# Optimization experiments

Hardware: AMD Instinct MI355X
Metric: run time of the kernel (lower is better)

Reference implementation:

```python
import jax, jax.numpy as jnp
import numpy as np

N_NODES = 50000
N_EDGES = 800000
IN_FEAT = 256
OUT_FEAT = 256
NUM_RELS = 8
ALPHA = 0.5


def setup_inputs() -> dict:
    key = jax.random.key(0)
    k1, k2, k3, k4, k5, k6 = jax.random.split(key, 6)
    x = jax.random.normal(k1, (N_NODES, IN_FEAT), dtype=jnp.float32)
    edge_index = jax.random.randint(k2, (2, N_EDGES), 0, N_NODES, dtype=jnp.int64)
    edge_type = jax.random.randint(k3, (N_EDGES,), 0, NUM_RELS, dtype=jnp.int64)
    # Xavier-uniform-ish init for weights (scale per fan-in/fan-out)
    gain = float(np.sqrt(2.0))  # calculate_gain('relu')
    lim_w = gain * float(np.sqrt(6.0 / (IN_FEAT + OUT_FEAT)))
    weight = jax.random.uniform(k4, (NUM_RELS, IN_FEAT, OUT_FEAT), dtype=jnp.float32,
                                minval=-lim_w, maxval=lim_w)
    loop_weight = jax.random.uniform(k5, (IN_FEAT, OUT_FEAT), dtype=jnp.float32,
                                     minval=-lim_w, maxval=lim_w)
    h_bias = jnp.zeros((OUT_FEAT,), dtype=jnp.float32)
    return {"edge_index": edge_index, "x": x, "edge_type": edge_type,
            "weight": weight, "h_bias": h_bias, "loop_weight": loop_weight}


def reference(edge_index, x, edge_type, weight, h_bias, loop_weight):
    num_nodes = x.shape[0]
    src, dst = edge_index[0], edge_index[1]
    # Per-edge message msg_e = x[src_e] @ weight[edge_type_e].
    # Computed efficiently as num_rels dense GEMMs over all nodes, then a fused
    # (relation, src) gather — identical math, avoids (E, in, out) weight blowup.
    hx = jnp.einsum('ni,rio->rno', x, weight)          # (R, N, out)
    msg = hx[edge_type, src]                            # (E, out)
    agg = jax.ops.segment_sum(msg, dst, num_segments=num_nodes)  # (N, out)
    node_repr = agg * jnp.asarray(ALPHA, x.dtype) ** 0.5
    node_repr = node_repr + h_bias
    loop_message = x @ loop_weight                      # (N, out)
    node_repr = node_repr + loop_message * jnp.asarray(1.0 - ALPHA, x.dtype) ** 0.5
    # activation=None, dropout=0.0 (eval) -> identity
    return node_repr
```

## Files before the change

### kernel.cpp

```cpp
#include <hip/hip_runtime.h>

typedef __bf16 bf16x8 __attribute__((ext_vector_type(8)));
typedef float f32x4 __attribute__((ext_vector_type(4)));

static __device__ __forceinline__ unsigned short f2bf(float f) {
    unsigned u = __builtin_bit_cast(unsigned, f);
    u += 0x7FFFu + ((u >> 16) & 1u);
    return (unsigned short)(u >> 16);
}
static __device__ __forceinline__ float bf2f(unsigned short h) {
    return __builtin_bit_cast(float, ((unsigned)h) << 16);
}

#define GLOAD_LDS16(g, l)                                              \
    __builtin_amdgcn_global_load_lds(                                  \
        (const __attribute__((address_space(1))) unsigned int*)(g),    \
        (__attribute__((address_space(3))) unsigned int*)(l), 16, 0, 0)

__global__ __launch_bounds__(256) void rgcn_zero(unsigned* __restrict__ p, int n) {
    int i = blockIdx.x * 256 + threadIdx.x;
    if (i < n) p[i] = 0;
}

__global__ __launch_bounds__(256) void rgcn_prep(const int* __restrict__ ei,
                                                 unsigned* __restrict__ cnt,
                                                 const float* __restrict__ x,
                                                 unsigned short* __restrict__ Z,
                                                 const float* __restrict__ w,
                                                 const float* __restrict__ lw,
                                                 unsigned short* __restrict__ wbT,
                                                 int E, int M, int HB, int CB) {
    const int b = blockIdx.x;
    const int t = threadIdx.x;
    if (b < HB) {
        int e = b * 256 + t;
        if (e < E) atomicAdd(&cnt[ei[E + e]], 1u);
    } else if (b < HB + CB) {
        int wv = ((b - HB) * 256 + t) >> 6;
        int lane = t & 63;
        if (wv < M) {
            float4 v = *(const float4*)(x + (size_t)wv * 256 + lane * 4);
            ushort4 o;
            o.x = f2bf(v.x); o.y = f2bf(v.y); o.z = f2bf(v.z); o.w = f2bf(v.w);
            *(ushort4*)(Z + (size_t)wv * 2304 + 2048 + lane * 4) = o;
        }
    } else {
        int bb = b - HB - CB;
        int kc = (bb % 9) * 256 + t;
        int n  = bb / 9;
        if (kc < 2304) {
            float v;
            if (kc < 2048) {
                int r = kc >> 8, k = kc & 255;
                v = w[((size_t)r * 256 + k) * 256 + n];
            } else {
                v = lw[(size_t)(kc - 2048) * 256 + n];
            }
            wbT[(size_t)n * 2304 + kc] = f2bf(v * 0.70710678118654752f);
        }
    }
}

__global__ __launch_bounds__(1024) void rgcn_scan1(const unsigned* __restrict__ cnt,
                                                   unsigned* __restrict__ off,
                                                   unsigned* __restrict__ bsum, int n) {
    __shared__ unsigned ws[16];
    const int t = threadIdx.x, lane = t & 63, wv = t >> 6;
    int i = blockIdx.x * 1024 + t;
    unsigned v = (i < n) ? cnt[i] : 0;
    unsigned s = v;
    #pragma unroll
    for (int d = 1; d < 64; d <<= 1) {
        unsigned u = __shfl_up(s, d, 64);
        if (lane >= d) s += u;
    }
    if (lane == 63) ws[wv] = s;
    __syncthreads();
    if (wv == 0) {
        unsigned b = (lane < 16) ? ws[lane] : 0;
        unsigned sb = b;
        #pragma unroll
        for (int d = 1; d < 16; d <<= 1) {
            unsigned u = __shfl_up(sb, d, 64);
            if (lane >= d) sb += u;
        }
        if (lane < 16) ws[lane] = sb - b;
        if (lane == 15) bsum[blockIdx.x] = sb;
    }
    __syncthreads();
    if (i < n) off[i] = ws[wv] + (s - v);
}

__global__ __launch_bounds__(64) void rgcn_scan2(unsigned* __restrict__ bsum,
                                                 unsigned* __restrict__ bsumo,
                                                 unsigned* __restrict__ off, int nb, int n) {
    const int lane = threadIdx.x & 63;
    unsigned b = (lane < nb) ? bsum[lane] : 0;
    unsigned s = b;
    #pragma unroll
    for (int d = 1; d < 64; d <<= 1) {
        unsigned u = __shfl_up(s, d, 64);
        if (lane >= d) s += u;
    }
    if (lane < nb) bsumo[lane] = s - b;
    if (lane == 63) off[n] = s;
}

__global__ __launch_bounds__(256) void rgcn_scan3(unsigned* __restrict__ off,
                                                  const unsigned* __restrict__ bsumo,
                                                  unsigned* __restrict__ cur, int n) {
    int i = blockIdx.x * 256 + threadIdx.x;
    if (i < n) {
        unsigned v = off[i] + bsumo[i >> 10];
        off[i] = v;
        cur[i] = v;
    }
}

__global__ __launch_bounds__(256) void rgcn_scatter(const int* __restrict__ ei,
                                                    const int* __restrict__ et,
                                                    unsigned* __restrict__ cur,
                                                    unsigned* __restrict__ recs, int E) {
    int e = blockIdx.x * 256 + threadIdx.x;
    if (e < E) {
        int dst = ei[E + e];
        unsigned p = atomicAdd(&cur[dst], 1u);
        recs[p] = (unsigned)ei[e] | ((unsigned)et[e] << 16);
    }
}

__global__ __launch_bounds__(256) void rgcn_agg(const unsigned* __restrict__ recs,
                                                const unsigned* __restrict__ off,
                                                unsigned short* __restrict__ Z, int M) {
    const int gw0  = (blockIdx.x * 256 + threadIdx.x) >> 6;
    const int nw   = (gridDim.x * 256) >> 6;
    const int lane = threadIdx.x & 63;
    const unsigned short* Zx = Z + 2048 + lane * 4;

#define GATHER(rr) (*(const ushort4*)(Zx + (size_t)((rr) & 0xFFFFu) * 2304))
#define ACCUM(rec, v_)                                                                 \
    {                                                                                  \
        f32x4 fv;                                                                      \
        fv[0] = bf2f(v_.x); fv[1] = bf2f(v_.y); fv[2] = bf2f(v_.z); fv[3] = bf2f(v_.w);\
        switch ((rec) >> 16) {                                                         \
            case 0: a0 += fv; break; case 1: a1 += fv; break;                          \
            case 2: a2 += fv; break; case 3: a3 += fv; break;                          \
            case 4: a4 += fv; break; case 5: a5 += fv; break;                          \
            case 6: a6 += fv; break; default: a7 += fv; break;                         \
        }                                                                              \
    }

    for (int w = gw0; w < M; w += nw) {
        const unsigned o0 = off[w], o1 = off[w + 1];
        f32x4 a0 = {}, a1 = {}, a2 = {}, a3 = {}, a4 = {}, a5 = {}, a6 = {}, a7 = {};

        for (unsigned base = o0; base < o1; base += 64) {
            const unsigned wdeg = (o1 - base < 64u) ? (o1 - base) : 64u;
            const unsigned myrec = ((unsigned)lane < wdeg) ? recs[base + lane] : 0u;

            unsigned j = 0;
            for (; j + 16 <= wdeg; j += 16) {
                unsigned rr[16];
                #pragma unroll
                for (int u = 0; u < 16; ++u) rr[u] = __shfl(myrec, (int)(j + u), 64);
                ushort4 vv[16];
                #pragma unroll
                for (int u = 0; u < 16; ++u) vv[u] = GATHER(rr[u]);
                #pragma unroll
                for (int u = 0; u < 16; ++u) ACCUM(rr[u], vv[u]);
            }
            for (; j + 4 <= wdeg; j += 4) {
                unsigned rr[4];
                #pragma unroll
                for (int u = 0; u < 4; ++u) rr[u] = __shfl(myrec, (int)(j + u), 64);
                ushort4 vv[4];
                #pragma unroll
                for (int u = 0; u < 4; ++u) vv[u] = GATHER(rr[u]);
                #pragma unroll
                for (int u = 0; u < 4; ++u) ACCUM(rr[u], vv[u]);
            }
            for (; j < wdeg; ++j) {
                unsigned r_ = __shfl(myrec, (int)j, 64);
                ushort4 v_ = GATHER(r_);
                ACCUM(r_, v_);
            }
        }

        unsigned short* zr = Z + (size_t)w * 2304 + lane * 4;
#define ST(rr_, ax)                                                                    \
        {                                                                              \
            ushort4 o_;                                                                \
            o_.x = f2bf(ax[0]); o_.y = f2bf(ax[1]);                                    \
            o_.z = f2bf(ax[2]); o_.w = f2bf(ax[3]);                                    \
            *(ushort4*)(zr + rr_ * 256) = o_;                                          \
        }
        ST(0, a0) ST(1, a1) ST(2, a2) ST(3, a3) ST(4, a4) ST(5, a5) ST(6, a6) ST(7, a7)
#undef ST
    }
#undef GATHER
#undef ACCUM
}

#define BM 64
#define BK 64
#define NCH 36

__global__ __launch_bounds__(256) void rgcn_gemm(
    const unsigned short* __restrict__ A,
    const unsigned short* __restrict__ Bt,
    float* __restrict__ out,
    const float* __restrict__ bias,
    int M)
{
    __shared__ char lds[8192 * 2 + 32768];
    char* Ab0 = lds;
    char* Ab1 = lds + 8192;
    char* Bb  = lds + 16384;

    const int tid  = threadIdx.x;
    const int lane = tid & 63;
    const int wid  = tid >> 6;
    const int wn   = wid * 64;
    const int m0   = blockIdx.x * BM;

    f32x4 acc[4][4] = {};

    auto stageA = [&](int chunk, char* dst) {
        #pragma unroll
        for (int it = 0; it < 2; ++it) {
            int o   = it * 4096 + tid * 16;
            int r   = o >> 7;
            int scb = (o & 127) ^ ((r & 7) << 4);
            int ga  = m0 + r; if (ga >= M) ga = M - 1;
            GLOAD_LDS16((const char*)A + (size_t)ga * 4608 + (size_t)chunk * 128 + scb, dst + o);
        }
    };
    auto stageB = [&](int chunk) {
        #pragma unroll
        for (int it = 0; it < 8; ++it) {
            int o   = it * 4096 + tid * 16;
            int r   = o >> 7;
            int scb = (o & 127) ^ ((r & 7) << 4);
            GLOAD_LDS16((const char*)Bt + (size_t)r * 4608 + (size_t)chunk * 128 + scb, Bb + o);
        }
    };

    stageA(0, Ab0);
    stageB(0);
    stageA(1, Ab1);
    asm volatile("s_waitcnt vmcnt(2)" ::: "memory");
    __builtin_amdgcn_s_barrier();
    __builtin_amdgcn_sched_barrier(0);

    for (int t = 0; t < NCH; ++t) {
        const char* Acur = (t & 1) ? Ab1 : Ab0;
        #pragma unroll
        for (int kk = 0; kk < 2; ++kk) {
            const int koff = kk * 32 + (lane >> 4) * 8;
            bf16x8 af[4], bfr[4];
            #pragma unroll
            for (int i = 0; i < 4; ++i) {
                int ar = i * 16 + (lane & 15);
                af[i] = *(const bf16x8*)(Acur + ((ar * 128 + koff * 2) ^ ((ar & 7) << 4)));
            }
            #pragma unroll
            for (int j = 0; j < 4; ++j) {
                int br = wn + j * 16 + (lane & 15);
                bfr[j] = *(const bf16x8*)(Bb + ((br * 128 + koff * 2) ^ ((br & 7) << 4)));
            }
            #pragma unroll
            for (int i = 0; i < 4; ++i)
                #pragma unroll
                for (int j = 0; j < 4; ++j)
                    acc[i][j] = __builtin_amdgcn_mfma_f32_16x16x32_bf16(af[i], bfr[j], acc[i][j], 0, 0, 0);
        }

        if (t < NCH - 1) {
            __builtin_amdgcn_s_barrier();
            __builtin_amdgcn_sched_barrier(0);
            stageB(t + 1);
            int tA = (t + 2 < NCH) ? t + 2 : NCH - 1;
            stageA(tA, (t & 1) ? Ab1 : Ab0);
            asm volatile("s_waitcnt vmcnt(2)" ::: "memory");
            __builtin_amdgcn_s_barrier();
            __builtin_amdgcn_sched_barrier(0);
        }
    }

    const int col = lane & 15;
    const int r0  = (lane >> 4) * 4;
    #pragma unroll
    for (int i = 0; i < 4; ++i) {
        #pragma unroll
        for (int j = 0; j < 4; ++j) {
            int gn = wn + j * 16 + col;
            float bv = bias[gn];
            #pragma unroll
            for (int rr = 0; rr < 4; ++rr) {
                int gm = m0 + i * 16 + r0 + rr;
                if (gm < M) out[(size_t)gm * 256 + gn] = acc[i][j][rr] + bv;
            }
        }
    }
}

extern "C" void kernel_launch(void* const* d_in, const int* in_sizes, int n_in,
                              void* d_out, int out_size, void* d_ws, size_t ws_size,
                              hipStream_t stream) {
    const int*   edge_index = (const int*)d_in[0];
    const float* x          = (const float*)d_in[1];
    const int*   edge_type  = (const int*)d_in[2];
    const float* weight     = (const float*)d_in[3];
    const float* h_bias     = (const float*)d_in[4];
    const float* loop_w     = (const float*)d_in[5];
    float* out = (float*)d_out;

    const int M = in_sizes[1] / 256;
    const int E = in_sizes[2];

    char* ws = (char*)d_ws;
    size_t off_b = 0;
    unsigned short* Zcat = (unsigned short*)(ws + off_b);
    off_b += (((size_t)M * 2304 * 2) + 255) & ~(size_t)255;
    unsigned short* wbT = (unsigned short*)(ws + off_b);
    off_b += (((size_t)256 * 2304 * 2) + 255) & ~(size_t)255;
    unsigned* cnt = (unsigned*)(ws + off_b);
    off_b += (((size_t)(M + 1) * 4) + 255) & ~(size_t)255;
    unsigned* off = (unsigned*)(ws + off_b);
    off_b += (((size_t)(M + 1) * 4) + 255) & ~(size_t)255;
    unsigned* bsum = (unsigned*)(ws + off_b);
    off_b += 256;
    unsigned* bsumo = (unsigned*)(ws + off_b);
    off_b += 256;
    unsigned* recs = (unsigned*)(ws + off_b);

    const int nb = (M + 1023) / 1024;
    const int HB = (E + 255) / 256;
    const int CB = (M + 3) / 4;

    rgcn_zero<<<(M + 255) / 256, 256, 0, stream>>>(cnt, M);
    rgcn_prep<<<HB + CB + 2304, 256, 0, stream>>>(edge_index, cnt, x, Zcat,
                                                  weight, loop_w, wbT, E, M, HB, CB);
    rgcn_scan1<<<nb, 1024, 0, stream>>>(cnt, off, bsum, M);
    rgcn_scan2<<<1, 64, 0, stream>>>(bsum, bsumo, off, nb, M);
    rgcn_scan3<<<(M + 255) / 256, 256, 0, stream>>>(off, bsumo, cnt, M);
    rgcn_scatter<<<(E + 255) / 256, 256, 0, stream>>>(edge_index, edge_type, cnt, recs, E);

    rgcn_agg<<<2560, 256, 0, stream>>>(recs, off, Zcat, M);

    rgcn_gemm<<<(M + BM - 1) / BM, 256, 0, stream>>>(Zcat, wbT, out, h_bias, M);
}
```

Baseline: 333.1 us.

## Fuse scan kernels into single-pass scan and enlarge GEMM tile to 256 rows

```diff
diff --git a/kernel.cpp b/kernel.cpp
--- a/kernel.cpp
+++ b/kernel.cpp
@@ -16,11 +16,6 @@
     __builtin_amdgcn_global_load_lds(                                  \
         (const __attribute__((address_space(1))) unsigned int*)(g),    \
         (__attribute__((address_space(3))) unsigned int*)(l), 16, 0, 0)
-
-__global__ __launch_bounds__(256) void rgcn_zero(unsigned* __restrict__ p, int n) {
-    int i = blockIdx.x * 256 + threadIdx.x;
-    if (i < n) p[i] = 0;
-}
 
 __global__ __launch_bounds__(256) void rgcn_prep(const int* __restrict__ ei,
                                                  unsigned* __restrict__ cnt,
@@ -61,12 +56,17 @@
     }
 }
 
-__global__ __launch_bounds__(1024) void rgcn_scan1(const unsigned* __restrict__ cnt,
-                                                   unsigned* __restrict__ off,
-                                                   unsigned* __restrict__ bsum, int n) {
-    __shared__ unsigned ws[16];
+__global__ __launch_bounds__(1024) void rgcn_scan_all(const unsigned* __restrict__ cnt,
+                                                      unsigned* __restrict__ off,
+                                                      unsigned* __restrict__ cur,
+                                                      unsigned* __restrict__ done,
+                                                      unsigned* __restrict__ bsum,
+                                                      int n, int nb) {
+    __shared__ unsigned wsum[16];
+    __shared__ unsigned bpre_s;
     const int t = threadIdx.x, lane = t & 63, wv = t >> 6;
-    int i = blockIdx.x * 1024 + t;
+    const int b = blockIdx.x;
+    int i = b * 1024 + t;
     unsigned v = (i < n) ? cnt[i] : 0;
     unsigned s = v;
     #pragma unroll
@@ -74,46 +74,45 @@
         unsigned u = __shfl_up(s, d, 64);
         if (lane >= d) s += u;
     }
-    if (lane == 63) ws[wv] = s;
+    if (lane == 63) wsum[wv] = s;
     __syncthreads();
     if (wv == 0) {
-        unsigned b = (lane < 16) ? ws[lane] : 0;
-        unsigned sb = b;
+        unsigned bb = (lane < 16) ? wsum[lane] : 0;
+        unsigned sb = bb;
         #pragma unroll
         for (int d = 1; d < 16; d <<= 1) {
             unsigned u = __shfl_up(sb, d, 64);
             if (lane >= d) sb += u;
         }
-        if (lane < 16) ws[lane] = sb - b;
-        if (lane == 15) bsum[blockIdx.x] = sb;
+        if (lane < 16) wsum[lane] = sb - bb;
+        if (lane == 15) {
+            atomicExch(&bsum[b], sb);
+            __threadfence();
+            atomicAdd(done, 1u);
+        }
     }
     __syncthreads();
-    if (i < n) off[i] = ws[wv] + (s - v);
-}
-
-__global__ __launch_bounds__(64) void rgcn_scan2(unsigned* __restrict__ bsum,
-                                                 unsigned* __restrict__ bsumo,
-                                                 unsigned* __restrict__ off, int nb, int n) {
-    const int lane = threadIdx.x & 63;
-    unsigned b = (lane < nb) ? bsum[lane] : 0;
-    unsigned s = b;
-    #pragma unroll
-    for (int d = 1; d < 64; d <<= 1) {
-        unsigned u = __shfl_up(s, d, 64);
-        if (lane >= d) s += u;
-    }
-    if (lane < nb) bsumo[lane] = s - b;
-    if (lane == 63) off[n] = s;
-}
-
-__global__ __launch_bounds__(256) void rgcn_scan3(unsigned* __restrict__ off,
-                                                  const unsigned* __restrict__ bsumo,
-                                                  unsigned* __restrict__ cur, int n) {
-    int i = blockIdx.x * 256 + threadIdx.x;
+    if (t == 0) {
+        while (atomicAdd(done, 0u) < (unsigned)nb) __builtin_amdgcn_s_sleep(8);
+    }
+    __syncthreads();
+    if (wv == 0) {
+        unsigned bv = (lane < nb) ? atomicAdd(&bsum[lane], 0u) : 0;
+        unsigned sp = bv;
+        #pragma unroll
+        for (int d = 1; d < 64; d <<= 1) {
+            unsigned u = __shfl_up(sp, d, 64);
+            if (lane >= d) sp += u;
+        }
+        if (lane == b) bpre_s = sp - bv;
+        if (b == 0 && lane == nb - 1) off[n] = sp;
+    }
+    __syncthreads();
+    unsigned base = bpre_s + wsum[wv];
     if (i < n) {
-        unsigned v = off[i] + bsumo[i >> 10];
-        off[i] = v;
-        cur[i] = v;
+        unsigned o = base + (s - v);
+        off[i] = o;
+        cur[i] = o;
     }
 }
 
@@ -201,103 +200,106 @@
 #undef ACCUM
 }
 
-#define BM 64
+#define BM 256
 #define BK 64
 #define NCH 36
 
-__global__ __launch_bounds__(256) void rgcn_gemm(
+__global__ __launch_bounds__(512) void rgcn_gemm(
     const unsigned short* __restrict__ A,
     const unsigned short* __restrict__ Bt,
     float* __restrict__ out,
     const float* __restrict__ bias,
     int M)
 {
-    __shared__ char lds[8192 * 2 + 32768];
+    __shared__ char lds[4 * 32768];
     char* Ab0 = lds;
-    char* Ab1 = lds + 8192;
-    char* Bb  = lds + 16384;
+    char* Ab1 = lds + 32768;
+    char* Bb0 = lds + 65536;
+    char* Bb1 = lds + 98304;
 
     const int tid  = threadIdx.x;
     const int lane = tid & 63;
     const int wid  = tid >> 6;
-    const int wn   = wid * 64;
+    const int wm   = (wid >> 1) * 64;
+    const int wn   = (wid & 1) * 128;
     const int m0   = blockIdx.x * BM;
 
-    f32x4 acc[4][4] = {};
+    f32x4 acc[4][8] = {};
 
     auto stageA = [&](int chunk, char* dst) {
         #pragma unroll
-        for (int it = 0; it < 2; ++it) {
-            int o   = it * 4096 + tid * 16;
+        for (int it = 0; it < 4; ++it) {
+            int o   = it * 8192 + tid * 16;
             int r   = o >> 7;
             int scb = (o & 127) ^ ((r & 7) << 4);
             int ga  = m0 + r; if (ga >= M) ga = M - 1;
             GLOAD_LDS16((const char*)A + (size_t)ga * 4608 + (size_t)chunk * 128 + scb, dst + o);
         }
     };
-    auto stageB = [&](int chunk) {
-        #pragma unroll
-        for (int it = 0; it < 8; ++it) {
-            int o   = it * 4096 + tid * 16;
+    auto stageB = [&](int chunk, char* dst) {
+        #pragma unroll
+        for (int it = 0; it < 4; ++it) {
+            int o   = it * 8192 + tid * 16;
             int r   = o >> 7;
             int scb = (o & 127) ^ ((r & 7) << 4);
-            GLOAD_LDS16((const char*)Bt + (size_t)r * 4608 + (size_t)chunk * 128 + scb, Bb + o);
+            GLOAD_LDS16((const char*)Bt + (size_t)r * 4608 + (size_t)chunk * 128 + scb, dst + o);
         }
     };
 
-    stageA(0, Ab0);
-    stageB(0);
-    stageA(1, Ab1);
-    asm volatile("s_waitcnt vmcnt(2)" ::: "memory");
+    stageA(0, Ab0); stageB(0, Bb0);
+    stageA(1, Ab1); stageB(1, Bb1);
+    asm volatile("s_waitcnt vmcnt(8)" ::: "memory");
     __builtin_amdgcn_s_barrier();
     __builtin_amdgcn_sched_barrier(0);
 
     for (int t = 0; t < NCH; ++t) {
-        const char* Acur = (t & 1) ? Ab1 : Ab0;
+        const char* Ac = (t & 1) ? Ab1 : Ab0;
+        const char* Bc = (t & 1) ? Bb1 : Bb0;
         #pragma unroll
         for (int kk = 0; kk < 2; ++kk) {
             const int koff = kk * 32 + (lane >> 4) * 8;
-            bf16x8 af[4], bfr[4];
+            bf16x8 af[4], bfr[8];
             #pragma unroll
             for (int i = 0; i < 4; ++i) {
-                int ar = i * 16 + (lane & 15);
-                af[i] = *(const bf16x8*)(Acur + ((ar * 128 + koff * 2) ^ ((ar & 7) << 4)));
+                int ar = wm + i * 16 + (lane & 15);
+                af[i] = *(const bf16x8*)(Ac + ((ar * 128 + koff * 2) ^ ((ar & 7) << 4)));
             }
             #pragma unroll
-            for (int j = 0; j < 4; ++j) {
+            for (int j = 0; j < 8; ++j) {
                 int br = wn + j * 16 + (lane & 15);
-                bfr[j] = *(const bf16x8*)(Bb + ((br * 128 + koff * 2) ^ ((br & 7) << 4)));
+                bfr[j] = *(const bf16x8*)(Bc + ((br * 128 + koff * 2) ^ ((br & 7) << 4)));
             }
             #pragma unroll
             for (int i = 0; i < 4; ++i)
                 #pragma unroll
-                for (int j = 0; j < 4; ++j)
+                for (int j = 0; j < 8; ++j)
                     acc[i][j] = __builtin_amdgcn_mfma_f32_16x16x32_bf16(af[i], bfr[j], acc[i][j], 0, 0, 0);
         }
 
         if (t < NCH - 1) {
             __builtin_amdgcn_s_barrier();
             __builtin_amdgcn_sched_barrier(0);
-            stageB(t + 1);
-            int tA = (t + 2 < NCH) ? t + 2 : NCH - 1;
-            stageA(tA, (t & 1) ? Ab1 : Ab0);
-            asm volatile("s_waitcnt vmcnt(2)" ::: "memory");
+            int tn = (t + 2 < NCH) ? t + 2 : NCH - 1;
+            stageA(tn, (t & 1) ? Ab1 : Ab0);
+            stageB(tn, (t & 1) ? Bb1 : Bb0);
+            asm volatile("s_waitcnt vmcnt(8)" ::: "memory");
             __builtin_amdgcn_s_barrier();
             __builtin_amdgcn_sched_barrier(0);
         }
     }
+    asm volatile("s_waitcnt vmcnt(0)" ::: "memory");
 
     const int col = lane & 15;
     const int r0  = (lane >> 4) * 4;
     #pragma unroll
     for (int i = 0; i < 4; ++i) {
         #pragma unroll
-        for (int j = 0; j < 4; ++j) {
+        for (int j = 0; j < 8; ++j) {
             int gn = wn + j * 16 + col;
             float bv = bias[gn];
             #pragma unroll
             for (int rr = 0; rr < 4; ++rr) {
-                int gm = m0 + i * 16 + r0 + rr;
+                int gm = m0 + wm + i * 16 + r0 + rr;
                 if (gm < M) out[(size_t)gm * 256 + gn] = acc[i][j][rr] + bv;
             }
         }
@@ -325,28 +327,27 @@
     unsigned short* wbT = (unsigned short*)(ws + off_b);
     off_b += (((size_t)256 * 2304 * 2) + 255) & ~(size_t)255;
     unsigned* cnt = (unsigned*)(ws + off_b);
-    off_b += (((size_t)(M + 1) * 4) + 255) & ~(size_t)255;
+    unsigned* done = cnt + M;
+    unsigned* bsum = cnt + M + 2;
+    off_b += (((size_t)(M + 2 + 64) * 4) + 255) & ~(size_t)255;
     unsigned* off = (unsigned*)(ws + off_b);
     off_b += (((size_t)(M + 1) * 4) + 255) & ~(size_t)255;
-    unsigned* bsum = (unsigned*)(ws + off_b);
-    off_b += 256;
-    unsigned* bsumo = (unsigned*)(ws + off_b);
-    off_b += 256;
+    unsigned* cur = (unsigned*)(ws + off_b);
+    off_b += (((size_t)M * 4) + 255) & ~(size_t)255;
     unsigned* recs = (unsigned*)(ws + off_b);
 
     const int nb = (M + 1023) / 1024;
     const int HB = (E + 255) / 256;
     const int CB = (M + 3) / 4;
 
-    rgcn_zero<<<(M + 255) / 256, 256, 0, stream>>>(cnt, M);
+    (void)hipMemsetAsync(cnt, 0, (size_t)(M + 2 + 64) * 4, stream);
+
     rgcn_prep<<<HB + CB + 2304, 256, 0, stream>>>(edge_index, cnt, x, Zcat,
                                                   weight, loop_w, wbT, E, M, HB, CB);
-    rgcn_scan1<<<nb, 1024, 0, stream>>>(cnt, off, bsum, M);
-    rgcn_scan2<<<1, 64, 0, stream>>>(bsum, bsumo, off, nb, M);
-    rgcn_scan3<<<(M + 255) / 256, 256, 0, stream>>>(off, bsumo, cnt, M);
-    rgcn_scatter<<<(E + 255) / 256, 256, 0, stream>>>(edge_index, edge_type, cnt, recs, E);
+    rgcn_scan_all<<<nb, 1024, 0, stream>>>(cnt, off, cur, done, bsum, M, nb);
+    rgcn_scatter<<<(E + 255) / 256, 256, 0, stream>>>(edge_index, edge_type, cur, recs, E);
 
     rgcn_agg<<<2560, 256, 0, stream>>>(recs, off, Zcat, M);
 
-    rgcn_gemm<<<(M + BM - 1) / BM, 256, 0, stream>>>(Zcat, wbT, out, h_bias, M);
-}
+    rgcn_gemm<<<(M + BM - 1) / BM, 512, 0, stream>>>(Zcat, wbT, out, h_bias, M);
+}
```

Result: faster. 311.5 us (-6.5%).
